# Kernel optimization log

Hardware: AMD Instinct MI355X
Metric: run time of the kernel (lower is better)

The kernel has to match this reference:

```python
import jax, jax.numpy as jnp
import numpy as np

N, E, FEAT, DIM, B = 200000, 1600000, 128, 64, 256


def setup_inputs() -> dict:
    key = jax.random.key(0)
    ks = jax.random.split(key, 16)
    s = 0.05
    x = jax.random.normal(ks[0], (N, FEAT), jnp.float32)
    edge_index = jax.random.randint(ks[1], (2, E), 0, N)
    batch = jnp.sort(jax.random.randint(ks[2], (N,), 0, B))
    return {
        'x': x,
        'edge_index': edge_index,
        'batch': batch,
        'lin0_w': jax.random.normal(ks[3], (FEAT, DIM), jnp.float32) * s,
        'lin0_b': jax.random.normal(ks[4], (DIM,), jnp.float32) * s,
        'conv_w': jax.random.normal(ks[5], (DIM, DIM), jnp.float32) * s,
        'conv_b': jax.random.normal(ks[6], (DIM,), jnp.float32) * s,
        'gru_w_ih': jax.random.normal(ks[7], (3 * DIM, DIM), jnp.float32) * s,
        'gru_w_hh': jax.random.normal(ks[8], (3 * DIM, DIM), jnp.float32) * s,
        'gru_b_ih': jax.random.normal(ks[9], (3 * DIM,), jnp.float32) * s,
        'gru_b_hh': jax.random.normal(ks[10], (3 * DIM,), jnp.float32) * s,
        'lstm_w_ih': jax.random.normal(ks[11], (4 * DIM, 2 * DIM), jnp.float32) * s,
        'lstm_w_hh': jax.random.normal(ks[12], (4 * DIM, DIM), jnp.float32) * s,
        'lstm_b_ih': jax.random.normal(ks[13], (4 * DIM,), jnp.float32) * s,
        'lstm_b_hh': jax.random.normal(ks[14], (4 * DIM,), jnp.float32) * s,
    }


def reference(x, edge_index, batch, lin0_w, lin0_b, conv_w, conv_b,
              gru_w_ih, gru_w_hh, gru_b_ih, gru_b_hh,
              lstm_w_ih, lstm_w_hh, lstm_b_ih, lstm_b_hh):
    n = x.shape[0]
    d = lin0_w.shape[1]
    # --- GCN normalization with self-loops (PyG gcn_norm, symmetric) ---
    loops = jnp.arange(n)
    row = jnp.concatenate([edge_index[0], loops])  # source nodes
    col = jnp.concatenate([edge_index[1], loops])  # target nodes
    deg = jax.ops.segment_sum(jnp.ones(row.shape, jnp.float32), col, num_segments=N)
    dinv = jnp.where(deg > 0, jax.lax.rsqrt(deg), 0.0)
    norm = dinv[row] * dinv[col]  # [E+N]

    out = jax.nn.relu(x @ lin0_w + lin0_b)  # [N, D]
    h = out  # GRU hidden (layer dim squeezed)
    feat = out
    for _ in range(3):
        # GCNConv: aggregate normalized neighbor messages
        hw = out @ conv_w                                   # [N, D]
        m = jax.ops.segment_sum(norm[:, None] * hw[row], col, num_segments=N) + conv_b
        m = jax.nn.relu(m)
        # torch.nn.GRU cell (gate order: reset, update, new)
        gi = m @ gru_w_ih.T + gru_b_ih
        gh = h @ gru_w_hh.T + gru_b_hh
        ir, iz, in_ = jnp.split(gi, 3, axis=-1)
        hr, hz, hn = jnp.split(gh, 3, axis=-1)
        r = jax.nn.sigmoid(ir + hr)
        z = jax.nn.sigmoid(iz + hz)
        ncand = jnp.tanh(in_ + r * hn)
        h = (1.0 - z) * ncand + z * h
        out = h
        feat = out

    # --- Set2Set pooling, processing_steps=3 (LSTM: 2D -> D) ---
    q_star = jnp.zeros((B, 2 * d), x.dtype)
    hl = jnp.zeros((B, d), x.dtype)
    cl = jnp.zeros((B, d), x.dtype)
    for _ in range(3):
        gates = q_star @ lstm_w_ih.T + lstm_b_ih + hl @ lstm_w_hh.T + lstm_b_hh
        i_, f_, g_, o_ = jnp.split(gates, 4, axis=-1)  # torch order i,f,g,o
        cl = jax.nn.sigmoid(f_) * cl + jax.nn.sigmoid(i_) * jnp.tanh(g_)
        hl = jax.nn.sigmoid(o_) * jnp.tanh(cl)
        q = hl                                             # [B, D]
        e = jnp.sum(out * q[batch], axis=-1)               # [N]
        emax = jax.ops.segment_max(e, batch, num_segments=B)
        a = jnp.exp(e - jax.lax.stop_gradient(emax)[batch])
        denom = jax.ops.segment_sum(a, batch, num_segments=B)
        a = a / denom[batch]                               # scatter-softmax
        r_read = jax.ops.segment_sum(a[:, None] * out, batch, num_segments=B)
        q_star = jnp.concatenate([q, r_read], axis=-1)     # [B, 2D]
    return (q_star, feat)
```

## Files before the change

kernel.cpp:

```cpp
#include <hip/hip_runtime.h>
#include <math.h>

#define FEATD 128
#define DIM 64
#define NB 256
#define SCB 256
#define KB 16
#define RNG 128
#define NBUCKMAX 2048
#define CH1 8192

typedef short bf16x8 __attribute__((ext_vector_type(8)));
typedef float f32x4 __attribute__((ext_vector_type(4)));

__device__ __forceinline__ float frcp_(float x){ return __builtin_amdgcn_rcpf(x); }
__device__ __forceinline__ float sigmoidf_(float x){ return frcp_(1.f+__expf(-x)); }
__device__ __forceinline__ float tanhf_(float x){ float e=__expf(2.f*x); return 1.f-2.f*frcp_(e+1.f); }

__device__ __forceinline__ unsigned short f2bf(float f){
  unsigned u = __float_as_uint(f);
  unsigned r = (u + 0x7FFFu + ((u>>16)&1u)) >> 16;
  return (unsigned short)r;
}
__device__ __forceinline__ float bf2f(unsigned short s){
  return __uint_as_float(((unsigned)s)<<16);
}

__device__ __forceinline__ int lower_bound_i(const int* __restrict__ a, int n, int key){
  int lo=0, hi=n;
  while(lo<hi){ int mid=(lo+hi)>>1; if(a[mid]<key) lo=mid+1; else hi=mid; }
  return lo;
}

__global__ void k_count(const int* __restrict__ col, int* __restrict__ deg, int E){
  int i=blockIdx.x*blockDim.x+threadIdx.x;
  if(i<E) atomicAdd(&deg[col[i]],1);
}

__global__ void k_dinv(const int* __restrict__ deg, float* __restrict__ dinv, int n){
  int i=blockIdx.x*blockDim.x+threadIdx.x;
  if(i<n) dinv[i]=rsqrtf((float)(deg[i]+1));
}

__global__ __launch_bounds__(256) void k_scan_part(const int* __restrict__ deg, int* __restrict__ part, int n){
  __shared__ int s[256];
  int b=blockIdx.x;
  int chunk=(n+SCB-1)/SCB;
  int lo=b*chunk, hi=min(lo+chunk,n);
  int acc=0;
  for(int i=lo+threadIdx.x;i<hi;i+=256) acc+=deg[i];
  s[threadIdx.x]=acc; __syncthreads();
  for(int off=128;off;off>>=1){
    if(threadIdx.x<off) s[threadIdx.x]+=s[threadIdx.x+off];
    __syncthreads();
  }
  if(threadIdx.x==0) part[b]=s[0];
}

__global__ __launch_bounds__(256) void k_scan_mid(int* __restrict__ part){
  __shared__ int s[256];
  int t=threadIdx.x;
  s[t]=part[t]; __syncthreads();
  for(int off=1;off<256;off<<=1){
    int v=(t>=off)? s[t-off]:0;
    __syncthreads();
    s[t]+=v;
    __syncthreads();
  }
  part[t]=(t>0)? s[t-1]:0;
}

__global__ __launch_bounds__(256) void k_scan_out(const int* __restrict__ deg, const int* __restrict__ part,
                                                  int* __restrict__ rp, int* __restrict__ gcur, int n){
  __shared__ int s[256];
  int b=blockIdx.x, t=threadIdx.x;
  int chunk=(n+SCB-1)/SCB;
  int lo=b*chunk, hi=min(lo+chunk,n);
  int tchunk=(chunk+255)/256;
  int tlo=lo+t*tchunk, thi=min(tlo+tchunk,hi);
  int acc=0;
  for(int i=tlo;i<thi;i++) acc+=deg[i];
  s[t]=acc; __syncthreads();
  for(int off=1;off<256;off<<=1){
    int v=(t>=off)? s[t-off]:0;
    __syncthreads();
    s[t]+=v;
    __syncthreads();
  }
  int pre=part[b]+((t>0)? s[t-1]:0);
  for(int i=tlo;i<thi;i++){
    rp[i]=pre;
    if((i&(RNG-1))==0) gcur[(i>>7)*32]=pre;
    pre+=deg[i];
  }
  if(b==SCB-1 && t==0) rp[n]=part[b]+s[255];
}

__global__ __launch_bounds__(256) void k_binscat(const int* __restrict__ row, const int* __restrict__ col,
                       int* __restrict__ gcur, unsigned* __restrict__ tmp, int E, int nbuck){
  __shared__ int lcnt[NBUCKMAX];
  __shared__ int lcur[NBUCKMAX];
  int t=threadIdx.x;
  for(int i=t;i<nbuck;i+=256) lcnt[i]=0;
  __syncthreads();
  int lo=blockIdx.x*CH1, hi=min(lo+CH1,E);
  for(int i=lo+t;i<hi;i+=256) atomicAdd(&lcnt[col[i]>>7],1);
  __syncthreads();
  for(int i=t;i<nbuck;i+=256){
    int cnt=lcnt[i];
    lcur[i]=(cnt>0)? atomicAdd(&gcur[i*32],cnt):0;
  }
  __syncthreads();
  for(int i=lo+t;i<hi;i+=256){
    int c=col[i], r=row[i];
    int pos=atomicAdd(&lcur[c>>7],1);
    tmp[pos]=((unsigned)r<<7)|(unsigned)(c&127);
  }
}

__global__ __launch_bounds__(256) void k_place(const unsigned* __restrict__ tmp, const int* __restrict__ rp,
                      const float* __restrict__ dinv, int2* __restrict__ epack, int n, int nbuck){
  __shared__ int lfill[RNG];
  __shared__ int lrp[RNG];
  __shared__ float ldv[RNG];
  int b=blockIdx.x, t=threadIdx.x;
  int nbase=b*RNG;
  int nn=min(RNG,n-nbase);
  if(t<nn){ lfill[t]=0; lrp[t]=rp[nbase+t]; ldv[t]=dinv[nbase+t]; }
  __syncthreads();
  int lo=rp[nbase], hi=rp[min(nbase+RNG,n)];
  for(int j=lo+t;j<hi;j+=256){
    unsigned v=tmp[j];
    int cl=v&127;
    int r=(int)(v>>7);
    int pos=atomicAdd(&lfill[cl],1);
    epack[lrp[cl]+pos]=make_int2(r,__float_as_int(dinv[r]*ldv[cl]));
  }
}

__global__ void k_prep_plain(const float* __restrict__ W, unsigned short* __restrict__ Bf, int K, int C){
  int i=blockIdx.x*blockDim.x+threadIdx.x;
  if(i>=K*C) return;
  int k=i/C, c=i%C;
  int t=c>>4, s=k>>5, lane=(c&15)|(((k>>3)&3)<<4), r=k&7;
  int S=K>>5;
  Bf[(((t*S)+s)*64+lane)*8+r]=f2bf(W[(size_t)k*C+c]);
}

__global__ void k_prep_gru(const float* __restrict__ wih, const float* __restrict__ whh,
                           unsigned short* __restrict__ Bf){
  int i=blockIdx.x*blockDim.x+threadIdx.x;
  if(i>=128*256) return;
  int k=i>>8, c=i&255;
  float v;
  if(c<128){
    v = (k<64) ? wih[c*64+k] : whh[c*64+(k-64)];
  } else if(c<192){
    v = (k<64) ? wih[c*64+k] : 0.f;
  } else {
    v = (k<64) ? 0.f : whh[(c-64)*64+(k-64)];
  }
  int t=c>>4, s=k>>5, lane=(c&15)|(((k>>3)&3)<<4), r=k&7;
  Bf[(((s*16)+t)*64+lane)*8+r]=f2bf(v);
}

__global__ __launch_bounds__(256) void k_lin0(const float* __restrict__ x, const unsigned short* __restrict__ Bf,
                      const float* __restrict__ bias,
                      unsigned short* __restrict__ hb, int ngrp){
  __shared__ __align__(16) unsigned short lt[4][16][72];
  int l=threadIdx.x&63, w=threadIdx.x>>6;
  int g=blockIdx.x*4+w;
  if(g>=ngrp) return;
  int row16=l&15, koff=(l>>4)*8, l16=l&15;
  f32x4 acc[4]={};
  const float* xr = x + (size_t)(g*16+row16)*128 + koff;
  #pragma unroll
  for(int s=0;s<4;s++){
    f32x4 a0=*(const f32x4*)(xr+s*32);
    f32x4 a1=*(const f32x4*)(xr+s*32+4);
    bf16x8 af;
    #pragma unroll
    for(int r=0;r<4;r++){ af[r]=(short)f2bf(a0[r]); af[4+r]=(short)f2bf(a1[r]); }
    #pragma unroll
    for(int t=0;t<4;t++){
      bf16x8 bf=*(const bf16x8*)(Bf+(((t*4)+s)*64+l)*8);
      acc[t]=__builtin_amdgcn_mfma_f32_16x16x32_bf16(af,bf,acc[t],0,0,0);
    }
  }
  #pragma unroll
  for(int t=0;t<4;t++){
    int c=t*16+l16;
    float b=bias[c];
    #pragma unroll
    for(int j=0;j<4;j++)
      lt[w][(l>>4)*4+j][c]=f2bf(fmaxf(acc[t][j]+b,0.f));
  }
  #pragma unroll
  for(int i=0;i<4;i++){
    int rl=i*4+(l>>4);
    uint2 v=*(const uint2*)&lt[w][rl][l16*4];
    ((uint2*)hb)[(((unsigned)(g*16+rl))<<4)+l16]=v;
  }
}

__global__ __launch_bounds__(256,4) void k_gruagg(
                     const unsigned short* __restrict__ hin, unsigned short* __restrict__ hout,
                     const int* __restrict__ rp, const int2* __restrict__ epack,
                     const float* __restrict__ dinv,
                     const unsigned short* __restrict__ Bcnv, const float* __restrict__ cb,
                     const unsigned short* __restrict__ Bgru,
                     const float* __restrict__ bih, const float* __restrict__ bhh,
                     float* __restrict__ h, int last, int ngrp, int n){
  __shared__ __align__(16) unsigned short Bs[8192];
  __shared__ __align__(16) unsigned short tAH[4][2][16][72];
  int tid=threadIdx.x;
  int l=tid&63, w=tid>>6;
  int g=blockIdx.x*4+w;
  bool act = g<ngrp;
  int gc = act? g : (ngrp-1);
  int q=l>>4, l16=l&15;
  int row16=l&15, koff=(l>>4)*8;

  unsigned short (*tA)[72] = tAH[w][0];
  unsigned short (*tH)[72] = tAH[w][1];

  bf16x8 bc[8];
  #pragma unroll
  for(int f=0;f<8;f++) bc[f]=*(const bf16x8*)(Bcnv+((size_t)f*64+l)*8);

  {
    const f32x4* gh=(const f32x4*)Bgru; f32x4* lh=(f32x4*)Bs;
    #pragma unroll
    for(int i=0;i<4;i++) lh[i*256+tid]=gh[i*256+tid];
  }

  const uint2* h64=(const uint2*)hin;
  #pragma unroll
  for(int rr=0;rr<4;rr++){
    int node=min(gc*16+rr*4+q, n-1);
    float a0=0.f,a1=0.f,a2=0.f,a3=0.f, b0=0.f,b1=0.f,b2=0.f,b3=0.f;
    int s=rp[node], e=rp[node+1];
    uint2 selfp=h64[((unsigned)node<<4)+l16];
    int j=s;
    for(; j+3<e; j+=4){
      int2 e0=epack[j];
      int2 e1=epack[j+1];
      int2 e2=epack[j+2];
      int2 e3=epack[j+3];
      uint2 p0=h64[((unsigned)e0.x<<4)+l16];
      uint2 p1=h64[((unsigned)e1.x<<4)+l16];
      uint2 p2=h64[((unsigned)e2.x<<4)+l16];
      uint2 p3=h64[((unsigned)e3.x<<4)+l16];
      float n0=__int_as_float(e0.y), n1=__int_as_float(e1.y);
      float n2=__int_as_float(e2.y), n3=__int_as_float(e3.y);
      a0+=n0*bf2f((unsigned short)p0.x); a1+=n0*bf2f((unsigned short)(p0.x>>16));
      a2+=n0*bf2f((unsigned short)p0.y); a3+=n0*bf2f((unsigned short)(p0.y>>16));
      b0+=n1*bf2f((unsigned short)p1.x); b1+=n1*bf2f((unsigned short)(p1.x>>16));
      b2+=n1*bf2f((unsigned short)p1.y); b3+=n1*bf2f((unsigned short)(p1.y>>16));
      a0+=n2*bf2f((unsigned short)p2.x); a1+=n2*bf2f((unsigned short)(p2.x>>16));
      a2+=n2*bf2f((unsigned short)p2.y); a3+=n2*bf2f((unsigned short)(p2.y>>16));
      b0+=n3*bf2f((unsigned short)p3.x); b1+=n3*bf2f((unsigned short)(p3.x>>16));
      b2+=n3*bf2f((unsigned short)p3.y); b3+=n3*bf2f((unsigned short)(p3.y>>16));
    }
    for(; j+1<e; j+=2){
      int2 e0=epack[j];
      int2 e1=epack[j+1];
      uint2 p0=h64[((unsigned)e0.x<<4)+l16];
      uint2 p1=h64[((unsigned)e1.x<<4)+l16];
      float n0=__int_as_float(e0.y), n1=__int_as_float(e1.y);
      a0+=n0*bf2f((unsigned short)p0.x); a1+=n0*bf2f((unsigned short)(p0.x>>16));
      a2+=n0*bf2f((unsigned short)p0.y); a3+=n0*bf2f((unsigned short)(p0.y>>16));
      b0+=n1*bf2f((unsigned short)p1.x); b1+=n1*bf2f((unsigned short)(p1.x>>16));
      b2+=n1*bf2f((unsigned short)p1.y); b3+=n1*bf2f((unsigned short)(p1.y>>16));
    }
    if(j<e){
      int2 e0=epack[j];
      uint2 p0=h64[((unsigned)e0.x<<4)+l16];
      float n0=__int_as_float(e0.y);
      a0+=n0*bf2f((unsigned short)p0.x); a1+=n0*bf2f((unsigned short)(p0.x>>16));
      a2+=n0*bf2f((unsigned short)p0.y); a3+=n0*bf2f((unsigned short)(p0.y>>16));
    }
    float dv=dinv[node]; dv*=dv;
    a0+=b0+dv*bf2f((unsigned short)selfp.x);
    a1+=b1+dv*bf2f((unsigned short)(selfp.x>>16));
    a2+=b2+dv*bf2f((unsigned short)selfp.y);
    a3+=b3+dv*bf2f((unsigned short)(selfp.y>>16));
    int ri=rr*4+q;
    unsigned* tAp=(unsigned*)&tA[ri][l16*4];
    tAp[0]=(unsigned)f2bf(a0)|(((unsigned)f2bf(a1))<<16);
    tAp[1]=(unsigned)f2bf(a2)|(((unsigned)f2bf(a3))<<16);
    unsigned* tHp=(unsigned*)&tH[ri][l16*4];
    tHp[0]=selfp.x; tHp[1]=selfp.y;
  }

  f32x4 accm[4]={};
  #pragma unroll
  for(int s=0;s<2;s++){
    bf16x8 af=*(const bf16x8*)&tA[row16][s*32+koff];
    #pragma unroll
    for(int t=0;t<4;t++)
      accm[t]=__builtin_amdgcn_mfma_f32_16x16x32_bf16(af,bc[t*2+s],accm[t],0,0,0);
  }
  #pragma unroll
  for(int t=0;t<4;t++){
    int c=t*16+l16;
    float b=cb[c];
    #pragma unroll
    for(int j=0;j<4;j++)
      tA[(l>>4)*4+j][c]=f2bf(fmaxf(accm[t][j]+b,0.f));
  }

  f32x4 acc[16]={};
  __syncthreads();
  #pragma unroll
  for(int s=0;s<4;s++){
    if(s>0){
      __syncthreads();
      const f32x4* gh=(const f32x4*)(Bgru+(size_t)s*8192); f32x4* lh=(f32x4*)Bs;
      #pragma unroll
      for(int i=0;i<4;i++) lh[i*256+tid]=gh[i*256+tid];
      __syncthreads();
    }
    bf16x8 af;
    if(s<2) af=*(const bf16x8*)&tA[row16][s*32+koff];
    else    af=*(const bf16x8*)&tH[row16][(s-2)*32+koff];
    #pragma unroll
    for(int t=0;t<16;t++){
      bf16x8 bf=*(const bf16x8*)(Bs+((size_t)t*64+l)*8);
      acc[t]=__builtin_amdgcn_mfma_f32_16x16x32_bf16(af,bf,acc[t],0,0,0);
    }
  }

  if(!act) return;
  float hn[16];
  #pragma unroll
  for(int t=0;t<4;t++){
    int d=t*16+l16;
    float br =bih[d]    +bhh[d];
    float bz =bih[64+d] +bhh[64+d];
    float bni=bih[128+d];
    float bnh=bhh[128+d];
    #pragma unroll
    for(int j=0;j<4;j++){
      float r  = sigmoidf_(acc[t][j]   + br);
      float z  = sigmoidf_(acc[4+t][j] + bz);
      float nc = tanhf_(acc[8+t][j] + bni + r*(acc[12+t][j] + bnh));
      float hold=bf2f(tH[(l>>4)*4+j][d]);
      hn[t*4+j]=(1.f-z)*nc + z*hold;
    }
  }
  #pragma unroll
  for(int t=0;t<4;t++){
    int d=t*16+l16;
    #pragma unroll
    for(int j=0;j<4;j++)
      tH[(l>>4)*4+j][d]=f2bf(hn[t*4+j]);
  }
  #pragma unroll
  for(int i=0;i<4;i++){
    int rl=i*4+(l>>4);
    uint2 v=*(const uint2*)&tH[rl][l16*4];
    ((uint2*)hout)[(((unsigned)(gc*16+rl))<<4)+l16]=v;
  }
  if(last){
    float* ft=(float*)&tAH[w][0][0][0];
    #pragma unroll
    for(int t=0;t<4;t++){
      int d=t*16+l16;
      #pragma unroll
      for(int j=0;j<4;j++)
        ft[((l>>4)*4+j)*68+d]=hn[t*4+j];
    }
    #pragma unroll
    for(int i=0;i<4;i++){
      int rl=i*4+(l>>4);
      f32x4 v=*(const f32x4*)&ft[rl*68+l16*4];
      *(f32x4*)&h[(size_t)(gc*16+rl)*64+l16*4]=v;
    }
  }
}

__global__ __launch_bounds__(256) void k_attn_part(const unsigned short* __restrict__ hb, const int* __restrict__ batch,
                        const float* __restrict__ hl, float* __restrict__ apart, int n){
  int b=blockIdx.x/KB, kb=blockIdx.x%KB;
  int tid=threadIdx.x, lane=tid&63, w=tid>>6;
  __shared__ float qs[64];
  __shared__ float wm[4], wsm[4];
  __shared__ float wacc[4][64];
  if(tid<64) qs[tid]=hl[b*64+tid];
  int lo=lower_bound_i(batch,n,b), hi=lower_bound_i(batch,n,b+1);
  int cnt=hi-lo;
  int chunk=(cnt+KB-1)/KB;
  int slo=lo+kb*chunk, shi=min(slo+chunk,hi);
  __syncthreads();
  float q=qs[lane];
  float mw=-3.0e38f, sw=0.f, aw=0.f;
  for(int i=slo+w;i<shi;i+=4){
    float f=bf2f(hb[(size_t)i*64+lane]);
    float v=f*q;
    #pragma unroll
    for(int off=32;off;off>>=1) v+=__shfl_xor(v,off);
    if(v>mw){
      float sc=__expf(mw-v);
      sw=sw*sc+1.f;
      aw=aw*sc+f;
      mw=v;
    } else {
      float p=__expf(v-mw);
      sw+=p;
      aw+=p*f;
    }
  }
  if(lane==0){ wm[w]=mw; wsm[w]=sw; }
  wacc[w][lane]=aw;
  __syncthreads();
  if(w==0){
    float M=fmaxf(fmaxf(wm[0],wm[1]),fmaxf(wm[2],wm[3]));
    float S=0.f, A=0.f;
    #pragma unroll
    for(int k=0;k<4;k++){
      float sc=__expf(wm[k]-M);
      S+=wsm[k]*sc;
      A+=wacc[k][lane]*sc;
    }
    float* p=apart+(size_t)blockIdx.x*68;
    p[lane]=A;
    if(lane==0){ p[64]=M; p[65]=S; }
  }
}

__global__ __launch_bounds__(256) void k_merge_lstm(const float* __restrict__ apart,
                   float* __restrict__ qstar, float* __restrict__ hl, float* __restrict__ cl,
                   const float* __restrict__ wih, const float* __restrict__ whh,
                   const float* __restrict__ bih, const float* __restrict__ bhh,
                   int do_merge, int do_lstm){
  int b=blockIdx.x, tid=threadIdx.x;
  __shared__ float qs[128];
  __shared__ float gates[256];
  if(do_merge){
    if(tid<64){
      const float* p0=apart+(size_t)b*KB*68;
      float M=-3.0e38f;
      #pragma unroll
      for(int k=0;k<KB;k++) M=fmaxf(M,p0[k*68+64]);
      float S=0.f, A=0.f;
      #pragma unroll
      for(int k=0;k<KB;k++){
        float sc=__expf(p0[k*68+64]-M);
        S+=p0[k*68+65]*sc;
        A+=p0[k*68+tid]*sc;
      }
      float inv=(S>0.f)? 1.f/S:0.f;
      float r=A*inv;
      qs[64+tid]=r;
      qstar[b*128+64+tid]=r;
    }
  } else {
    if(tid<64) qs[64+tid]=qstar[b*128+64+tid];
  }
  if(tid<64) qs[tid]=hl[b*64+tid];
  __syncthreads();
  if(!do_lstm) return;
  float acc=bih[tid]+bhh[tid];
  const float* wi=wih+(size_t)tid*128;
  #pragma unroll 8
  for(int k=0;k<128;k++) acc+=qs[k]*wi[k];
  const float* w2=whh+(size_t)tid*64;
  #pragma unroll 8
  for(int k=0;k<64;k++) acc+=qs[k]*w2[k];
  gates[tid]=acc;
  __syncthreads();
  if(tid<64){
    float i_=gates[tid], f_=gates[64+tid], g_=gates[128+tid], o_=gates[192+tid];
    float c=sigmoidf_(f_)*cl[b*64+tid]+sigmoidf_(i_)*tanhf(g_);
    float hn=sigmoidf_(o_)*tanhf(c);
    cl[b*64+tid]=c; hl[b*64+tid]=hn;
    qstar[b*128+tid]=hn;
  }
}

extern "C" void kernel_launch(void* const* d_in, const int* in_sizes, int n_in,
                              void* d_out, int out_size, void* d_ws, size_t ws_size,
                              hipStream_t stream){
  const float* x      =(const float*)d_in[0];
  const int*   ei     =(const int*)d_in[1];
  const int*   batch  =(const int*)d_in[2];
  const float* lin0_w =(const float*)d_in[3];
  const float* lin0_b =(const float*)d_in[4];
  const float* conv_w =(const float*)d_in[5];
  const float* conv_b =(const float*)d_in[6];
  const float* gwih   =(const float*)d_in[7];
  const float* gwhh   =(const float*)d_in[8];
  const float* gbih   =(const float*)d_in[9];
  const float* gbhh   =(const float*)d_in[10];
  const float* lwih   =(const float*)d_in[11];
  const float* lwhh   =(const float*)d_in[12];
  const float* lbih   =(const float*)d_in[13];
  const float* lbhh   =(const float*)d_in[14];

  int N = in_sizes[0]/FEATD;
  int E = in_sizes[1]/2;
  const int* row = ei;
  const int* col = ei + E;

  float* qstar = (float*)d_out;
  float* h     = (float*)d_out + NB*2*DIM;

  char* ws=(char*)d_ws;
  size_t off=0;
  auto alloc=[&](size_t bytes)->void*{ void* p=ws+off; off=(off+bytes+255)&~(size_t)255; return p; };
  int*   deg  =(int*)  alloc((size_t)N*4);
  float* dinv =(float*)alloc((size_t)N*4);
  int*   rp   =(int*)  alloc((size_t)(N+1)*4);
  int*   part =(int*)  alloc((size_t)SCB*4);
  int*   gcur =(int*)  alloc((size_t)NBUCKMAX*32*4);
  unsigned* tmp=(unsigned*)alloc((size_t)E*4);
  int2*  epack=(int2*) alloc((size_t)E*8);
  unsigned short* hb0  =(unsigned short*)alloc((size_t)N*64*2);
  unsigned short* hb1  =(unsigned short*)alloc((size_t)N*64*2);
  float* hl   =(float*)alloc((size_t)NB*DIM*4);
  float* cl   =(float*)alloc((size_t)NB*DIM*4);
  float* apart=(float*)alloc((size_t)NB*KB*68*4);
  unsigned short* Bgru =(unsigned short*)alloc(128*256*2);
  unsigned short* Blin =(unsigned short*)alloc(128*64*2);
  unsigned short* Bcnv =(unsigned short*)alloc(64*64*2);

  hipMemsetAsync(deg ,0,(size_t)N*4,stream);
  hipMemsetAsync(hl  ,0,(size_t)NB*DIM*4,stream);
  hipMemsetAsync(cl  ,0,(size_t)NB*DIM*4,stream);
  hipMemsetAsync(qstar,0,(size_t)NB*2*DIM*4,stream);

  int nbuck=(N+RNG-1)/RNG;

  k_count<<<(E+255)/256,256,0,stream>>>(col,deg,E);
  k_dinv <<<(N+255)/256,256,0,stream>>>(deg,dinv,N);
  k_scan_part<<<SCB,256,0,stream>>>(deg,part,N);
  k_scan_mid <<<1,256,0,stream>>>(part);
  k_scan_out <<<SCB,256,0,stream>>>(deg,part,rp,gcur,N);
  k_binscat<<<(E+CH1-1)/CH1,256,0,stream>>>(row,col,gcur,tmp,E,nbuck);
  k_place<<<nbuck,256,0,stream>>>(tmp,rp,dinv,epack,N,nbuck);

  k_prep_plain<<<(128*64+255)/256,256,0,stream>>>(lin0_w,Blin,128,64);
  k_prep_plain<<<(64*64+255)/256,256,0,stream>>>(conv_w,Bcnv,64,64);
  k_prep_gru  <<<(128*256+255)/256,256,0,stream>>>(gwih,gwhh,Bgru);

  int ngrp=(N+15)/16;
  int gb=(ngrp+3)/4;

  k_lin0<<<gb,256,0,stream>>>(x,Blin,lin0_b,hb0,ngrp);

  k_gruagg<<<gb,256,0,stream>>>(hb0,hb1,rp,epack,dinv,Bcnv,conv_b,Bgru,gbih,gbhh,h,0,ngrp,N);
  k_gruagg<<<gb,256,0,stream>>>(hb1,hb0,rp,epack,dinv,Bcnv,conv_b,Bgru,gbih,gbhh,h,0,ngrp,N);
  k_gruagg<<<gb,256,0,stream>>>(hb0,hb1,rp,epack,dinv,Bcnv,conv_b,Bgru,gbih,gbhh,h,1,ngrp,N);

  k_merge_lstm<<<NB,256,0,stream>>>(apart,qstar,hl,cl,lwih,lwhh,lbih,lbhh,0,1);
  for(int st=0;st<3;st++){
    k_attn_part<<<NB*KB,256,0,stream>>>(hb1,batch,hl,apart,N);
    int do_lstm = (st<2)? 1:0;
    k_merge_lstm<<<NB,256,0,stream>>>(apart,qstar,hl,cl,lwih,lwhh,lbih,lbhh,1,do_lstm);
  }
}
```

Before: 550.7 us.

## Reorder GRU weight layout and compute gates per output column tile

```diff
diff --git a/kernel.cpp b/kernel.cpp
--- a/kernel.cpp
+++ b/kernel.cpp
@@ -161,7 +161,8 @@
     v = (k<64) ? 0.f : whh[(c-64)*64+(k-64)];
   }
   int t=c>>4, s=k>>5, lane=(c&15)|(((k>>3)&3)<<4), r=k&7;
-  Bf[(((s*16)+t)*64+lane)*8+r]=f2bf(v);
+  int j=t&3, gate=t>>2;
+  Bf[(((j*16)+(gate*4)+s)*64+lane)*8+r]=f2bf(v);
 }
 
 __global__ __launch_bounds__(256) void k_lin0(const float* __restrict__ x, const unsigned short* __restrict__ Bf,
@@ -223,16 +224,6 @@
 
   unsigned short (*tA)[72] = tAH[w][0];
   unsigned short (*tH)[72] = tAH[w][1];
-
-  bf16x8 bc[8];
-  #pragma unroll
-  for(int f=0;f<8;f++) bc[f]=*(const bf16x8*)(Bcnv+((size_t)f*64+l)*8);
-
-  {
-    const f32x4* gh=(const f32x4*)Bgru; f32x4* lh=(f32x4*)Bs;
-    #pragma unroll
-    for(int i=0;i<4;i++) lh[i*256+tid]=gh[i*256+tid];
-  }
 
   const uint2* h64=(const uint2*)hin;
   #pragma unroll
@@ -293,62 +284,66 @@
     tHp[0]=selfp.x; tHp[1]=selfp.y;
   }
 
-  f32x4 accm[4]={};
-  #pragma unroll
-  for(int s=0;s<2;s++){
-    bf16x8 af=*(const bf16x8*)&tA[row16][s*32+koff];
-    #pragma unroll
-    for(int t=0;t<4;t++)
-      accm[t]=__builtin_amdgcn_mfma_f32_16x16x32_bf16(af,bc[t*2+s],accm[t],0,0,0);
-  }
-  #pragma unroll
-  for(int t=0;t<4;t++){
-    int c=t*16+l16;
-    float b=cb[c];
-    #pragma unroll
-    for(int j=0;j<4;j++)
-      tA[(l>>4)*4+j][c]=f2bf(fmaxf(accm[t][j]+b,0.f));
-  }
-
-  f32x4 acc[16]={};
-  __syncthreads();
-  #pragma unroll
-  for(int s=0;s<4;s++){
-    if(s>0){
-      __syncthreads();
-      const f32x4* gh=(const f32x4*)(Bgru+(size_t)s*8192); f32x4* lh=(f32x4*)Bs;
+  {
+    bf16x8 bc[8];
+    #pragma unroll
+    for(int f=0;f<8;f++) bc[f]=*(const bf16x8*)(Bcnv+((size_t)f*64+l)*8);
+    f32x4 accm[4]={};
+    #pragma unroll
+    for(int s=0;s<2;s++){
+      bf16x8 af=*(const bf16x8*)&tA[row16][s*32+koff];
+      #pragma unroll
+      for(int t=0;t<4;t++)
+        accm[t]=__builtin_amdgcn_mfma_f32_16x16x32_bf16(af,bc[t*2+s],accm[t],0,0,0);
+    }
+    #pragma unroll
+    for(int t=0;t<4;t++){
+      int c=t*16+l16;
+      float b=cb[c];
+      #pragma unroll
+      for(int j=0;j<4;j++)
+        tA[(l>>4)*4+j][c]=f2bf(fmaxf(accm[t][j]+b,0.f));
+    }
+  }
+
+  float hn[16];
+  #pragma unroll
+  for(int jt=0;jt<4;jt++){
+    __syncthreads();
+    {
+      const f32x4* gh=(const f32x4*)(Bgru+(size_t)jt*8192); f32x4* lh=(f32x4*)Bs;
       #pragma unroll
       for(int i=0;i<4;i++) lh[i*256+tid]=gh[i*256+tid];
-      __syncthreads();
-    }
-    bf16x8 af;
-    if(s<2) af=*(const bf16x8*)&tA[row16][s*32+koff];
-    else    af=*(const bf16x8*)&tH[row16][(s-2)*32+koff];
-    #pragma unroll
-    for(int t=0;t<16;t++){
-      bf16x8 bf=*(const bf16x8*)(Bs+((size_t)t*64+l)*8);
-      acc[t]=__builtin_amdgcn_mfma_f32_16x16x32_bf16(af,bf,acc[t],0,0,0);
-    }
-  }
-
-  if(!act) return;
-  float hn[16];
-  #pragma unroll
-  for(int t=0;t<4;t++){
-    int d=t*16+l16;
+    }
+    __syncthreads();
+    f32x4 acc[4]={};
+    #pragma unroll
+    for(int s=0;s<4;s++){
+      bf16x8 af;
+      if(s<2) af=*(const bf16x8*)&tA[row16][s*32+koff];
+      else    af=*(const bf16x8*)&tH[row16][(s-2)*32+koff];
+      #pragma unroll
+      for(int gt=0;gt<4;gt++){
+        bf16x8 bf=*(const bf16x8*)(Bs+((size_t)(gt*4+s)*64+l)*8);
+        acc[gt]=__builtin_amdgcn_mfma_f32_16x16x32_bf16(af,bf,acc[gt],0,0,0);
+      }
+    }
+    int d=jt*16+l16;
     float br =bih[d]    +bhh[d];
     float bz =bih[64+d] +bhh[64+d];
     float bni=bih[128+d];
     float bnh=bhh[128+d];
     #pragma unroll
-    for(int j=0;j<4;j++){
-      float r  = sigmoidf_(acc[t][j]   + br);
-      float z  = sigmoidf_(acc[4+t][j] + bz);
-      float nc = tanhf_(acc[8+t][j] + bni + r*(acc[12+t][j] + bnh));
-      float hold=bf2f(tH[(l>>4)*4+j][d]);
-      hn[t*4+j]=(1.f-z)*nc + z*hold;
-    }
-  }
+    for(int jj=0;jj<4;jj++){
+      float r  = sigmoidf_(acc[0][jj] + br);
+      float z  = sigmoidf_(acc[1][jj] + bz);
+      float nc = tanhf_(acc[2][jj] + bni + r*(acc[3][jj] + bnh));
+      float hold=bf2f(tH[(l>>4)*4+jj][d]);
+      hn[jt*4+jj]=(1.f-z)*nc + z*hold;
+    }
+  }
+
+  if(!act) return;
   #pragma unroll
   for(int t=0;t<4;t++){
     int d=t*16+l16;
```

Result: slower. 579.7 us (+5.3%).
